# Performance work log

Hardware: AMD Instinct MI355X
Metric: run time of the kernel (lower is better)

Reference implementation:

```python
import jax, jax.numpy as jnp
import numpy as np

N = 50000      # nodes
E = 800000     # edges (avg degree 16)
D = 128        # d_model
H = 8          # num_heads
DK = D // H    # d_k = 16


def setup_inputs() -> dict:
    key = jax.random.key(0)
    ks = jax.random.split(key, 9)
    scale = np.float32(1.0 / np.sqrt(D))
    return {
        "q": jax.random.normal(ks[0], (N, D), jnp.float32),
        "k": jax.random.normal(ks[1], (N, D), jnp.float32),
        "v": jax.random.normal(ks[2], (N, D), jnp.float32),
        "e": jax.random.normal(ks[3], (E, D), jnp.float32),
        "src": jax.random.randint(ks[4], (E,), 0, N),
        "dst": jax.random.randint(ks[5], (E,), 0, N),
        # nn.Linear(D, D, bias=False) weights, stored as [in, out]
        "Wq": jax.random.normal(ks[6], (D, D), jnp.float32) * scale,
        "Wk": jax.random.normal(ks[7], (D, D), jnp.float32) * scale,
        "Wv": jax.random.normal(ks[8], (D, D), jnp.float32) * scale,
    }


def reference(q, k, v, e, src, dst, Wq, Wk, Wv):
    inv_sqrt_dk = np.float32(1.0 / np.sqrt(DK))
    # node-level V projection, then per-edge gather of src V  -> [E, H, DK]
    Vn = (v @ Wv).reshape(N, H, DK)
    Ve = Vn[src]
    # per-edge Q from dst node, K from (src k + edge feature e)
    Qe = (q[dst] @ Wq).reshape(E, H, DK)
    Ke = ((k[src] + e) @ Wk).reshape(E, H, DK)
    # per-edge HxH score matrix: Q @ K^T / sqrt(d_k), leaky-relu
    s = jnp.einsum("ehd,egd->ehg", Qe, Ke) * inv_sqrt_dk   # [E, H, H]
    s = jax.nn.leaky_relu(s)
    # softmax over last head axis (within each edge, as in reduce_func dim=-1)
    A = jax.nn.softmax(s, axis=-1)
    # per-edge message, heads regrouped -> [E, D]
    He = jnp.einsum("ehg,egd->ehd", A, Ve).reshape(E, D)
    # plain sum over incoming edges per destination node -> [N, D]
    return jax.ops.segment_sum(He, dst, num_segments=N)
```

## Files before the change

kernel.cpp:

```cpp
#include <hip/hip_runtime.h>
#include <hip/hip_bf16.h>
#include <math.h>

#define NN 50000
#define EE 800000
#define DD 128
#define HH 8
#define DKK 16

typedef __attribute__((ext_vector_type(8))) short short8;
typedef __attribute__((ext_vector_type(4))) float f32x4;
typedef __attribute__((ext_vector_type(4))) unsigned short ushort4v;
typedef __attribute__((ext_vector_type(8))) unsigned short ushort8v;

static __device__ __forceinline__ unsigned short f2bf(float x) {
  __hip_bfloat16 h = __float2bfloat16(x);
  return *reinterpret_cast<unsigned short*>(&h);
}
static __device__ __forceinline__ float bf2f(unsigned short u) {
  return __uint_as_float(((unsigned int)u) << 16);
}

__global__ __launch_bounds__(256) void hist_kernel(const int* __restrict__ dst,
                                                   int* __restrict__ cnt) {
  int i4 = blockIdx.x * 256 + threadIdx.x;
  if (i4 < EE / 4) {
    int4 d = *(const int4*)&dst[i4 * 4];
    atomicAdd(&cnt[d.x], 1);
    atomicAdd(&cnt[d.y], 1);
    atomicAdd(&cnt[d.z], 1);
    atomicAdd(&cnt[d.w], 1);
  }
}

#define SCAN_NB ((NN + 1023) / 1024)

__global__ __launch_bounds__(256) void scan1_kernel(const int* __restrict__ cnt,
                                                    int* __restrict__ bsum) {
  __shared__ int red[256];
  const int b = blockIdx.x, t = threadIdx.x;
  const int base = b * 1024 + t * 4;
  int s = 0;
  if (base + 3 < NN) {
    int4 v = *(const int4*)&cnt[base];
    s = v.x + v.y + v.z + v.w;
  } else {
    for (int j = 0; j < 4; ++j) if (base + j < NN) s += cnt[base + j];
  }
  red[t] = s;
  __syncthreads();
  for (int off = 1; off < 256; off <<= 1) {
    int v = (t >= off) ? red[t - off] : 0;
    __syncthreads();
    red[t] += v;
    __syncthreads();
  }
  if (t == 255) bsum[b] = red[255];
}

__global__ __launch_bounds__(256) void scan3_kernel(const int* __restrict__ cnt,
                                                    const int* __restrict__ bsum,
                                                    int* __restrict__ rowptr) {
  __shared__ int red[256];
  __shared__ int bs[SCAN_NB];
  const int b = blockIdx.x, t = threadIdx.x;
  if (t < SCAN_NB) bs[t] = bsum[t];
  const int base = b * 1024 + t * 4;
  int v0 = 0, v1 = 0, v2 = 0, v3 = 0;
  if (base + 3 < NN) {
    int4 v = *(const int4*)&cnt[base];
    v0 = v.x; v1 = v.y; v2 = v.z; v3 = v.w;
  } else {
    if (base + 0 < NN) v0 = cnt[base + 0];
    if (base + 1 < NN) v1 = cnt[base + 1];
    if (base + 2 < NN) v2 = cnt[base + 2];
    if (base + 3 < NN) v3 = cnt[base + 3];
  }
  red[t] = v0 + v1 + v2 + v3;
  __syncthreads();
  for (int off = 1; off < 256; off <<= 1) {
    int v = (t >= off) ? red[t - off] : 0;
    __syncthreads();
    red[t] += v;
    __syncthreads();
  }
  int bpre = 0;
  for (int j = 0; j < b; ++j) bpre += bs[j];
  int r = bpre + ((t == 0) ? 0 : red[t - 1]);
  if (base + 0 < NN) { rowptr[base + 0] = r; r += v0; }
  if (base + 1 < NN) { rowptr[base + 1] = r; r += v1; }
  if (base + 2 < NN) { rowptr[base + 2] = r; r += v2; }
  if (base + 3 < NN) { rowptr[base + 3] = r; }
}

__global__ __launch_bounds__(256) void fill_kernel(const int* __restrict__ dst,
                                                   const int* __restrict__ rowptr,
                                                   int* __restrict__ cur,
                                                   int* __restrict__ perm) {
  int i4 = blockIdx.x * 256 + threadIdx.x;
  if (i4 < EE / 4) {
    int4 dv = *(const int4*)&dst[i4 * 4];
    int d0 = dv.x, d1 = dv.y, d2 = dv.z, d3 = dv.w;
    int s0 = atomicAdd(&cur[d0], 1); perm[rowptr[d0] + s0] = i4 * 4 + 0;
    int s1 = atomicAdd(&cur[d1], 1); perm[rowptr[d1] + s1] = i4 * 4 + 1;
    int s2 = atomicAdd(&cur[d2], 1); perm[rowptr[d2] + s2] = i4 * 4 + 2;
    int s3 = atomicAdd(&cur[d3], 1); perm[rowptr[d3] + s3] = i4 * 4 + 3;
  }
}

__global__ void prep_w_kernel(const float* __restrict__ Wq,
                              const float* __restrict__ Wk,
                              const float* __restrict__ Wv,
                              unsigned short* __restrict__ WqT,
                              unsigned short* __restrict__ WkT,
                              unsigned short* __restrict__ WvT) {
  int c = blockIdx.x & 127;
  int m = blockIdx.x >> 7;
  int j = threadIdx.x;
  const float* W = (m == 0) ? Wq : (m == 1) ? Wk : Wv;
  unsigned short* o = (m == 0) ? WqT : (m == 1) ? WkT : WvT;
  o[j * DD + c] = f2bf(W[c * DD + j]);
}

__global__ __launch_bounds__(512) void node_proj_kernel(
    const float* __restrict__ q, const float* __restrict__ v,
    const float* __restrict__ k,
    const unsigned short* __restrict__ WqT, const unsigned short* __restrict__ WvT,
    unsigned short* __restrict__ Qh, unsigned short* __restrict__ Vh,
    unsigned short* __restrict__ kh)
{
  __shared__ __align__(16) unsigned short xl[64 * 136];
  const int tid = threadIdx.x;
  const int n0 = blockIdx.x * 64;

  #pragma unroll
  for (int p = 0; p < 2; ++p) {
    int f = p * 512 + tid;
    int i = f >> 4, c8 = f & 15;
    int n = n0 + i;
    if (n < NN) {
      float4 a = *(const float4*)&k[(size_t)n * DD + c8 * 8];
      float4 b = *(const float4*)&k[(size_t)n * DD + c8 * 8 + 4];
      ushort8v o = { f2bf(a.x), f2bf(a.y), f2bf(a.z), f2bf(a.w),
                     f2bf(b.x), f2bf(b.y), f2bf(b.z), f2bf(b.w) };
      *(ushort8v*)&kh[(size_t)n * DD + c8 * 8] = o;
    }
  }

  for (int m = 0; m < 2; ++m) {
    const float* x = m ? v : q;
    const unsigned short* WT = m ? WvT : WqT;
    unsigned short* o = m ? Vh : Qh;

    __syncthreads();
    #pragma unroll
    for (int p = 0; p < 4; ++p) {
      int f = p * 512 + tid;
      int i = f >> 5, c4 = f & 31;
      int n = n0 + i;
      float4 t = (n < NN) ? *(const float4*)&x[(size_t)n * DD + c4 * 4]
                          : float4{0.f, 0.f, 0.f, 0.f};
      ushort4v u = { f2bf(t.x), f2bf(t.y), f2bf(t.z), f2bf(t.w) };
      *(ushort4v*)&xl[i * 136 + c4 * 4] = u;
    }
    __syncthreads();

    const int lane = tid & 63, wid = tid >> 6;
    const int rg = wid & 3, cg = wid >> 2;
    const int lr = lane & 15, lg = lane >> 4;

    f32x4 acc0 = {0.f,0.f,0.f,0.f}, acc1 = {0.f,0.f,0.f,0.f};
    f32x4 acc2 = {0.f,0.f,0.f,0.f}, acc3 = {0.f,0.f,0.f,0.f};

    const unsigned short* Ab = &xl[(rg * 16 + lr) * 136];
    const unsigned short* B0 = &WT[(size_t)(cg * 64 +  0 + lr) * DD];
    const unsigned short* B1 = &WT[(size_t)(cg * 64 + 16 + lr) * DD];
    const unsigned short* B2 = &WT[(size_t)(cg * 64 + 32 + lr) * DD];
    const unsigned short* B3 = &WT[(size_t)(cg * 64 + 48 + lr) * DD];

    #pragma unroll
    for (int kk = 0; kk < 4; ++kk) {
      const int kof = kk * 32 + lg * 8;
      short8 a = *(const short8*)(Ab + kof);
      acc0 = __builtin_amdgcn_mfma_f32_16x16x32_bf16(a, *(const short8*)(B0 + kof), acc0, 0, 0, 0);
      acc1 = __builtin_amdgcn_mfma_f32_16x16x32_bf16(a, *(const short8*)(B1 + kof), acc1, 0, 0, 0);
      acc2 = __builtin_amdgcn_mfma_f32_16x16x32_bf16(a, *(const short8*)(B2 + kof), acc2, 0, 0, 0);
      acc3 = __builtin_amdgcn_mfma_f32_16x16x32_bf16(a, *(const short8*)(B3 + kof), acc3, 0, 0, 0);
    }

    const int r0 = rg * 16 + lg * 4;
    const int cb = cg * 64 + lr;
    #pragma unroll
    for (int r = 0; r < 4; ++r) {
      int n = n0 + r0 + r;
      if (n < NN) {
        unsigned short* orow = &o[(size_t)n * DD + cb];
        orow[ 0] = f2bf(acc0[r]);
        orow[16] = f2bf(acc1[r]);
        orow[32] = f2bf(acc2[r]);
        orow[48] = f2bf(acc3[r]);
      }
    }
  }
}

__global__ __launch_bounds__(512) void edge_attn_kernel(
    const unsigned short* __restrict__ kh, const float* __restrict__ e,
    const int* __restrict__ src, const int* __restrict__ dst,
    const int* __restrict__ perm,
    const unsigned short* __restrict__ WkT,
    const unsigned short* __restrict__ Qh, const unsigned short* __restrict__ Vh,
    float* __restrict__ out)
{
  __shared__ __align__(16) unsigned short buf[64 * 136];
  __shared__ __align__(16) unsigned short vbuf[64 * 136];
  __shared__ __align__(16) unsigned short pbuf[8 * 16 * 24];
  __shared__ int s_perm[64], s_src[64], s_dst[64];

  const int tid = threadIdx.x;
  const size_t e0 = (size_t)blockIdx.x * 64;
  const int lane = tid & 63, wid = tid >> 6;
  const int lr = lane & 15, lg = lane >> 4;

  if (tid < 64) {
    int pe = perm[e0 + tid];
    s_perm[tid] = pe;
    s_src[tid] = src[pe];
    s_dst[tid] = dst[pe];
  }
  __syncthreads();

  #pragma unroll
  for (int p = 0; p < 2; ++p) {
    int f = p * 512 + tid;
    int i2 = f >> 4, c8 = f & 15;
    ushort8v vv = *(const ushort8v*)&Vh[(size_t)s_src[i2] * DD + c8 * 8];
    ushort8v kv = *(const ushort8v*)&kh[(size_t)s_src[i2] * DD + c8 * 8];
    const float* ep = &e[(size_t)s_perm[i2] * DD + c8 * 8];
    float4 ea = *(const float4*)ep;
    float4 eb = *(const float4*)(ep + 4);
    *(ushort8v*)&vbuf[i2 * 136 + c8 * 8] = vv;
    ushort8v o;
    o[0] = f2bf(bf2f(kv[0]) + ea.x);
    o[1] = f2bf(bf2f(kv[1]) + ea.y);
    o[2] = f2bf(bf2f(kv[2]) + ea.z);
    o[3] = f2bf(bf2f(kv[3]) + ea.w);
    o[4] = f2bf(bf2f(kv[4]) + eb.x);
    o[5] = f2bf(bf2f(kv[5]) + eb.y);
    o[6] = f2bf(bf2f(kv[6]) + eb.z);
    o[7] = f2bf(bf2f(kv[7]) + eb.w);
    *(ushort8v*)&buf[i2 * 136 + c8 * 8] = o;
  }

  const short8 zero8 = {0, 0, 0, 0, 0, 0, 0, 0};
  const int ebase = wid * 8;
  short8 qf[4];
  #pragma unroll
  for (int j = 0; j < 4; ++j) {
    if (lg < 2) {
      int ie = ebase + 2 * j + (lr >> 3);
      qf[j] = *(const short8*)&Qh[(size_t)s_dst[ie] * DD + (lr & 7) * DKK + lg * 8];
    } else qf[j] = zero8;
  }
  __syncthreads();

  {
    const int rg = wid & 3, cg = wid >> 2;

    f32x4 a0 = {0.f,0.f,0.f,0.f}, a1 = {0.f,0.f,0.f,0.f};
    f32x4 a2 = {0.f,0.f,0.f,0.f}, a3 = {0.f,0.f,0.f,0.f};

    const unsigned short* Ab = &buf[(rg * 16 + lr) * 136];
    const unsigned short* B0 = &WkT[(size_t)(cg * 64 +  0 + lr) * DD];
    const unsigned short* B1 = &WkT[(size_t)(cg * 64 + 16 + lr) * DD];
    const unsigned short* B2 = &WkT[(size_t)(cg * 64 + 32 + lr) * DD];
    const unsigned short* B3 = &WkT[(size_t)(cg * 64 + 48 + lr) * DD];

    #pragma unroll
    for (int kk = 0; kk < 4; ++kk) {
      const int kof = kk * 32 + lg * 8;
      short8 a = *(const short8*)(Ab + kof);
      a0 = __builtin_amdgcn_mfma_f32_16x16x32_bf16(a, *(const short8*)(B0 + kof), a0, 0, 0, 0);
      a1 = __builtin_amdgcn_mfma_f32_16x16x32_bf16(a, *(const short8*)(B1 + kof), a1, 0, 0, 0);
      a2 = __builtin_amdgcn_mfma_f32_16x16x32_bf16(a, *(const short8*)(B2 + kof), a2, 0, 0, 0);
      a3 = __builtin_amdgcn_mfma_f32_16x16x32_bf16(a, *(const short8*)(B3 + kof), a3, 0, 0, 0);
    }

    __syncthreads();

    const int r0 = rg * 16 + lg * 4;
    const int cb = cg * 64 + lr;
    #pragma unroll
    for (int r = 0; r < 4; ++r) {
      buf[(r0 + r) * 136 + cb +  0] = f2bf(a0[r]);
      buf[(r0 + r) * 136 + cb + 16] = f2bf(a1[r]);
      buf[(r0 + r) * 136 + cb + 32] = f2bf(a2[r]);
      buf[(r0 + r) * 136 + cb + 48] = f2bf(a3[r]);
    }
  }
  __syncthreads();

  {
    const bool valid = ((lr < 8) == (lg < 2));
    unsigned short* pb = &pbuf[wid * 16 * 24];

    #pragma unroll
    for (int j = 0; j < 4; ++j) {
      const int iea = ebase + 2 * j, ieb = iea + 1;

      short8 af = zero8;
      if (lg < 2) {
        int ie = (lr < 8) ? iea : ieb;
        af = *(const short8*)&buf[ie * 136 + (lr & 7) * DKK + lg * 8];
      }
      f32x4 c = {0.f, 0.f, 0.f, 0.f};
      c = __builtin_amdgcn_mfma_f32_16x16x32_bf16(af, qf[j], c, 0, 0, 0);

      float s0, s1, s2, s3;
      {
        float x0 = c[0] * 0.25f, x1 = c[1] * 0.25f;
        float x2 = c[2] * 0.25f, x3 = c[3] * 0.25f;
        x0 = (x0 >= 0.f) ? x0 : 0.01f * x0;
        x1 = (x1 >= 0.f) ? x1 : 0.01f * x1;
        x2 = (x2 >= 0.f) ? x2 : 0.01f * x2;
        x3 = (x3 >= 0.f) ? x3 : 0.01f * x3;
        s0 = valid ? x0 : -1e30f;
        s1 = valid ? x1 : -1e30f;
        s2 = valid ? x2 : -1e30f;
        s3 = valid ? x3 : -1e30f;
      }
      float m = fmaxf(fmaxf(s0, s1), fmaxf(s2, s3));
      m = fmaxf(m, __shfl_xor(m, 16));
      m = fmaxf(m, __shfl_xor(m, 32));
      float p0 = __expf(s0 - m), p1 = __expf(s1 - m);
      float p2 = __expf(s2 - m), p3 = __expf(s3 - m);
      float su = p0 + p1 + p2 + p3;
      su += __shfl_xor(su, 16);
      su += __shfl_xor(su, 32);
      float rs = 1.0f / su;

      ushort4v pk = { f2bf(p0 * rs), f2bf(p1 * rs), f2bf(p2 * rs), f2bf(p3 * rs) };
      *(ushort4v*)&pb[lr * 24 + lg * 4] = pk;

      short8 pa = zero8;
      if (lg < 2) pa = *(const short8*)&pb[lr * 24 + lg * 8];
      short8 vf = zero8;
      if (lg < 2) {
        const unsigned short* vr = &vbuf[(lg ? ieb : iea) * 136 + lr];
        vf[0] = (short)vr[0 * 16];
        vf[1] = (short)vr[1 * 16];
        vf[2] = (short)vr[2 * 16];
        vf[3] = (short)vr[3 * 16];
        vf[4] = (short)vr[4 * 16];
        vf[5] = (short)vr[5 * 16];
        vf[6] = (short)vr[6 * 16];
        vf[7] = (short)vr[7 * 16];
      }
      f32x4 hc = {0.f, 0.f, 0.f, 0.f};
      hc = __builtin_amdgcn_mfma_f32_16x16x32_bf16(pa, vf, hc, 0, 0, 0);

      #pragma unroll
      for (int r = 0; r < 4; ++r) {
        int rr = lg * 4 + r;
        int ie = (rr < 8) ? iea : ieb;
        buf[ie * 136 + (rr & 7) * DKK + lr] = f2bf(hc[r]);
      }
    }
  }

  {
    const int d2 = lane;
    float s0 = 0.0f, s1 = 0.0f;
    int curd = s_dst[ebase];
    #pragma unroll 8
    for (int j = 0; j < 8; ++j) {
      int i2 = ebase + j;
      int dn2 = s_dst[i2];
      if (dn2 != curd) {
        atomicAdd(&out[(size_t)curd * DD + d2 * 2],     s0);
        atomicAdd(&out[(size_t)curd * DD + d2 * 2 + 1], s1);
        s0 = 0.0f; s1 = 0.0f;
        curd = dn2;
      }
      unsigned int w = *(const unsigned int*)&buf[i2 * 136 + d2 * 2];
      s0 += bf2f((unsigned short)(w & 0xffff));
      s1 += bf2f((unsigned short)(w >> 16));
    }
    atomicAdd(&out[(size_t)curd * DD + d2 * 2],     s0);
    atomicAdd(&out[(size_t)curd * DD + d2 * 2 + 1], s1);
  }
}

extern "C" void kernel_launch(void* const* d_in, const int* in_sizes, int n_in,
                              void* d_out, int out_size, void* d_ws, size_t ws_size,
                              hipStream_t stream) {
  const float* q  = (const float*)d_in[0];
  const float* k  = (const float*)d_in[1];
  const float* v  = (const float*)d_in[2];
  const float* e  = (const float*)d_in[3];
  const int*   src = (const int*)d_in[4];
  const int*   dst = (const int*)d_in[5];
  const float* Wq = (const float*)d_in[6];
  const float* Wk = (const float*)d_in[7];
  const float* Wv = (const float*)d_in[8];

  float* out = (float*)d_out;
  char* wsb = (char*)d_ws;
  unsigned short* Qh  = (unsigned short*)wsb;
  unsigned short* Vh  = Qh + (size_t)NN * DD;
  unsigned short* kh  = Vh + (size_t)NN * DD;
  unsigned short* WqT = kh + (size_t)NN * DD;
  unsigned short* WkT = WqT + DD * DD;
  unsigned short* WvT = WkT + DD * DD;
  int* cnt    = (int*)(WvT + DD * DD);
  int* cur    = cnt + NN;
  int* rowptr = cur + NN;
  int* bsum   = rowptr + NN + 1;
  int* perm   = bsum + 64;

  hipMemsetAsync(d_out, 0, (size_t)NN * DD * sizeof(float), stream);
  hipMemsetAsync(cnt, 0, 2 * NN * sizeof(int), stream);

  hist_kernel <<<(EE / 4 + 255) / 256, 256, 0, stream>>>(dst, cnt);
  scan1_kernel<<<SCAN_NB, 256, 0, stream>>>(cnt, bsum);
  scan3_kernel<<<SCAN_NB, 256, 0, stream>>>(cnt, bsum, rowptr);
  fill_kernel <<<(EE / 4 + 255) / 256, 256, 0, stream>>>(dst, rowptr, cur, perm);

  prep_w_kernel<<<3 * DD, DD, 0, stream>>>(Wq, Wk, Wv, WqT, WkT, WvT);
  node_proj_kernel<<<(NN + 63) / 64, 512, 0, stream>>>(q, v, k, WqT, WvT,
                                                       Qh, Vh, kh);
  edge_attn_kernel<<<EE / 64, 512, 0, stream>>>(kh, e, src, dst, perm,
                                                WkT, Qh, Vh, out);
}
```

Measured before the change: 416.2 us.

## Stage edge features via direct global-to-LDS loads and read V straight from global

Edge feature rows are now copied into a shared-memory float buffer with global_load_lds, so the bulk e traffic bypasses registers. The k loads and Q fragment loads are issued before the barrier so they overlap with that transfer. The V staging buffer is removed and V fragments are gathered directly from global memory in the attention step. The final segment reduction now has each thread handle one column over 16 edges after a new barrier, which changes the granularity of the atomic adds. In exchange, LDS use rises with the fp32 e buffer, and the direct V gathers are strided 2-byte global reads.

```diff
diff --git a/kernel.cpp b/kernel.cpp
--- a/kernel.cpp
+++ b/kernel.cpp
@@ -19,6 +19,12 @@
 }
 static __device__ __forceinline__ float bf2f(unsigned short u) {
   return __uint_as_float(((unsigned int)u) << 16);
+}
+
+static __device__ __forceinline__ void gload_lds16(void* lds, const void* g) {
+  __builtin_amdgcn_global_load_lds(
+      (const __attribute__((address_space(1))) unsigned int*)g,
+      (__attribute__((address_space(3))) unsigned int*)lds, 16, 0, 0);
 }
 
 __global__ __launch_bounds__(256) void hist_kernel(const int* __restrict__ dst,
@@ -213,7 +219,7 @@
     float* __restrict__ out)
 {
   __shared__ __align__(16) unsigned short buf[64 * 136];
-  __shared__ __align__(16) unsigned short vbuf[64 * 136];
+  __shared__ __align__(16) float ebuf[64 * 128];
   __shared__ __align__(16) unsigned short pbuf[8 * 16 * 24];
   __shared__ int s_perm[64], s_src[64], s_dst[64];
 
@@ -231,15 +237,40 @@
   __syncthreads();
 
   #pragma unroll
-  for (int p = 0; p < 2; ++p) {
-    int f = p * 512 + tid;
-    int i2 = f >> 4, c8 = f & 15;
-    ushort8v vv = *(const ushort8v*)&Vh[(size_t)s_src[i2] * DD + c8 * 8];
-    ushort8v kv = *(const ushort8v*)&kh[(size_t)s_src[i2] * DD + c8 * 8];
-    const float* ep = &e[(size_t)s_perm[i2] * DD + c8 * 8];
-    float4 ea = *(const float4*)ep;
-    float4 eb = *(const float4*)(ep + 4);
-    *(ushort8v*)&vbuf[i2 * 136 + c8 * 8] = vv;
+  for (int t = 0; t < 4; ++t) {
+    int ew = (wid << 3) + (t << 1) + (lane >> 5);
+    const float* gp = &e[(size_t)s_perm[ew] * DD + (lane & 31) * 4];
+    gload_lds16(&ebuf[wid * 1024 + t * 256], gp);
+  }
+
+  ushort8v kvv[2];
+  #pragma unroll
+  for (int j = 0; j < 2; ++j) {
+    int flat = j * 512 + tid;
+    kvv[j] = *(const ushort8v*)&kh[(size_t)s_src[flat >> 4] * DD + (flat & 15) * 8];
+  }
+
+  const short8 zero8 = {0, 0, 0, 0, 0, 0, 0, 0};
+  const int ebase = wid * 8;
+  short8 qf[4];
+  #pragma unroll
+  for (int j = 0; j < 4; ++j) {
+    if (lg < 2) {
+      int ie = ebase + 2 * j + (lr >> 3);
+      qf[j] = *(const short8*)&Qh[(size_t)s_dst[ie] * DD + (lr & 7) * DKK + lg * 8];
+    } else qf[j] = zero8;
+  }
+  __syncthreads();
+
+  #pragma unroll
+  for (int j = 0; j < 2; ++j) {
+    int flat = j * 512 + tid;
+    int i2 = flat >> 4, c8 = flat & 15;
+    int we = i2 >> 3, j2 = i2 & 7;
+    const float* ef = &ebuf[we * 1024 + (j2 >> 1) * 256 + (j2 & 1) * 128 + c8 * 8];
+    float4 ea = *(const float4*)ef;
+    float4 eb = *(const float4*)(ef + 4);
+    ushort8v kv = kvv[j];
     ushort8v o;
     o[0] = f2bf(bf2f(kv[0]) + ea.x);
     o[1] = f2bf(bf2f(kv[1]) + ea.y);
@@ -250,17 +281,6 @@
     o[6] = f2bf(bf2f(kv[6]) + eb.z);
     o[7] = f2bf(bf2f(kv[7]) + eb.w);
     *(ushort8v*)&buf[i2 * 136 + c8 * 8] = o;
-  }
-
-  const short8 zero8 = {0, 0, 0, 0, 0, 0, 0, 0};
-  const int ebase = wid * 8;
-  short8 qf[4];
-  #pragma unroll
-  for (int j = 0; j < 4; ++j) {
-    if (lg < 2) {
-      int ie = ebase + 2 * j + (lr >> 3);
-      qf[j] = *(const short8*)&Qh[(size_t)s_dst[ie] * DD + (lr & 7) * DKK + lg * 8];
-    } else qf[j] = zero8;
   }
   __syncthreads();
 
@@ -346,7 +366,7 @@
       if (lg < 2) pa = *(const short8*)&pb[lr * 24 + lg * 8];
       short8 vf = zero8;
       if (lg < 2) {
-        const unsigned short* vr = &vbuf[(lg ? ieb : iea) * 136 + lr];
+        const unsigned short* vr = &Vh[(size_t)s_src[lg ? ieb : iea] * DD + lr];
         vf[0] = (short)vr[0 * 16];
         vf[1] = (short)vr[1 * 16];
         vf[2] = (short)vr[2 * 16];
@@ -367,27 +387,25 @@
       }
     }
   }
+  __syncthreads();
 
   {
-    const int d2 = lane;
-    float s0 = 0.0f, s1 = 0.0f;
-    int curd = s_dst[ebase];
+    const int c = tid >> 7, d2 = tid & 127;
+    const int base = c * 16;
+    float s = 0.0f;
+    int curd = s_dst[base];
     #pragma unroll 8
-    for (int j = 0; j < 8; ++j) {
-      int i2 = ebase + j;
+    for (int j = 0; j < 16; ++j) {
+      int i2 = base + j;
       int dn2 = s_dst[i2];
       if (dn2 != curd) {
-        atomicAdd(&out[(size_t)curd * DD + d2 * 2],     s0);
-        atomicAdd(&out[(size_t)curd * DD + d2 * 2 + 1], s1);
-        s0 = 0.0f; s1 = 0.0f;
+        atomicAdd(&out[(size_t)curd * DD + d2], s);
+        s = 0.0f;
         curd = dn2;
       }
-      unsigned int w = *(const unsigned int*)&buf[i2 * 136 + d2 * 2];
-      s0 += bf2f((unsigned short)(w & 0xffff));
-      s1 += bf2f((unsigned short)(w >> 16));
-    }
-    atomicAdd(&out[(size_t)curd * DD + d2 * 2],     s0);
-    atomicAdd(&out[(size_t)curd * DD + d2 * 2 + 1], s1);
+      s += bf2f(buf[i2 * 136 + d2]);
+    }
+    atomicAdd(&out[(size_t)curd * DD + d2], s);
   }
 }
 
```

After: 493.6 us. +18.6%, slower.

## Make edge attention wave-local: each wave owns 16 edges, drop shared staging

Applied to the files above, without the earlier changes.

The edge attention kernel now runs 256 threads, and each of its 4 waves owns 16 edges end to end. Each wave loads k+e straight from global into MFMA A-fragments and computes all 128 output columns of the K projection with 8 accumulators. The V staging buffer is removed, and V fragments are gathered directly from global memory in the score/message stage. This removes shared-memory staging and two block barriers and roughly halves LDS use, which should raise occupancy. In exchange it raises register pressure, gives uncoalesced strided global V reads, and makes each wave read the full WkT.

```diff
diff --git a/kernel.cpp b/kernel.cpp
--- a/kernel.cpp
+++ b/kernel.cpp
@@ -204,7 +204,7 @@
   }
 }
 
-__global__ __launch_bounds__(512) void edge_attn_kernel(
+__global__ __launch_bounds__(256) void edge_attn_kernel(
     const unsigned short* __restrict__ kh, const float* __restrict__ e,
     const int* __restrict__ src, const int* __restrict__ dst,
     const int* __restrict__ perm,
@@ -213,14 +213,14 @@
     float* __restrict__ out)
 {
   __shared__ __align__(16) unsigned short buf[64 * 136];
-  __shared__ __align__(16) unsigned short vbuf[64 * 136];
-  __shared__ __align__(16) unsigned short pbuf[8 * 16 * 24];
+  __shared__ __align__(16) unsigned short pbuf[4 * 16 * 24];
   __shared__ int s_perm[64], s_src[64], s_dst[64];
 
   const int tid = threadIdx.x;
   const size_t e0 = (size_t)blockIdx.x * 64;
   const int lane = tid & 63, wid = tid >> 6;
   const int lr = lane & 15, lg = lane >> 4;
+  const int ebase = wid * 16;
 
   if (tid < 64) {
     int pe = perm[e0 + tid];
@@ -230,82 +230,60 @@
   }
   __syncthreads();
 
+  const short8 zero8 = {0, 0, 0, 0, 0, 0, 0, 0};
+  short8 qf[8];
   #pragma unroll
-  for (int p = 0; p < 2; ++p) {
-    int f = p * 512 + tid;
-    int i2 = f >> 4, c8 = f & 15;
-    ushort8v vv = *(const ushort8v*)&Vh[(size_t)s_src[i2] * DD + c8 * 8];
-    ushort8v kv = *(const ushort8v*)&kh[(size_t)s_src[i2] * DD + c8 * 8];
-    const float* ep = &e[(size_t)s_perm[i2] * DD + c8 * 8];
-    float4 ea = *(const float4*)ep;
-    float4 eb = *(const float4*)(ep + 4);
-    *(ushort8v*)&vbuf[i2 * 136 + c8 * 8] = vv;
-    ushort8v o;
-    o[0] = f2bf(bf2f(kv[0]) + ea.x);
-    o[1] = f2bf(bf2f(kv[1]) + ea.y);
-    o[2] = f2bf(bf2f(kv[2]) + ea.z);
-    o[3] = f2bf(bf2f(kv[3]) + ea.w);
-    o[4] = f2bf(bf2f(kv[4]) + eb.x);
-    o[5] = f2bf(bf2f(kv[5]) + eb.y);
-    o[6] = f2bf(bf2f(kv[6]) + eb.z);
-    o[7] = f2bf(bf2f(kv[7]) + eb.w);
-    *(ushort8v*)&buf[i2 * 136 + c8 * 8] = o;
-  }
-
-  const short8 zero8 = {0, 0, 0, 0, 0, 0, 0, 0};
-  const int ebase = wid * 8;
-  short8 qf[4];
-  #pragma unroll
-  for (int j = 0; j < 4; ++j) {
+  for (int j = 0; j < 8; ++j) {
     if (lg < 2) {
       int ie = ebase + 2 * j + (lr >> 3);
       qf[j] = *(const short8*)&Qh[(size_t)s_dst[ie] * DD + (lr & 7) * DKK + lg * 8];
     } else qf[j] = zero8;
   }
-  __syncthreads();
 
   {
-    const int rg = wid & 3, cg = wid >> 2;
-
-    f32x4 a0 = {0.f,0.f,0.f,0.f}, a1 = {0.f,0.f,0.f,0.f};
-    f32x4 a2 = {0.f,0.f,0.f,0.f}, a3 = {0.f,0.f,0.f,0.f};
-
-    const unsigned short* Ab = &buf[(rg * 16 + lr) * 136];
-    const unsigned short* B0 = &WkT[(size_t)(cg * 64 +  0 + lr) * DD];
-    const unsigned short* B1 = &WkT[(size_t)(cg * 64 + 16 + lr) * DD];
-    const unsigned short* B2 = &WkT[(size_t)(cg * 64 + 32 + lr) * DD];
-    const unsigned short* B3 = &WkT[(size_t)(cg * 64 + 48 + lr) * DD];
+    const int prow = s_perm[ebase + lr];
+    const int srow = s_src[ebase + lr];
+    const unsigned short* khp = &kh[(size_t)srow * DD];
+    const float* ep = &e[(size_t)prow * DD];
+
+    f32x4 acc[8];
+    #pragma unroll
+    for (int c = 0; c < 8; ++c) acc[c] = f32x4{0.f, 0.f, 0.f, 0.f};
 
     #pragma unroll
     for (int kk = 0; kk < 4; ++kk) {
       const int kof = kk * 32 + lg * 8;
-      short8 a = *(const short8*)(Ab + kof);
-      a0 = __builtin_amdgcn_mfma_f32_16x16x32_bf16(a, *(const short8*)(B0 + kof), a0, 0, 0, 0);
-      a1 = __builtin_amdgcn_mfma_f32_16x16x32_bf16(a, *(const short8*)(B1 + kof), a1, 0, 0, 0);
-      a2 = __builtin_amdgcn_mfma_f32_16x16x32_bf16(a, *(const short8*)(B2 + kof), a2, 0, 0, 0);
-      a3 = __builtin_amdgcn_mfma_f32_16x16x32_bf16(a, *(const short8*)(B3 + kof), a3, 0, 0, 0);
-    }
-
-    __syncthreads();
-
-    const int r0 = rg * 16 + lg * 4;
-    const int cb = cg * 64 + lr;
-    #pragma unroll
-    for (int r = 0; r < 4; ++r) {
-      buf[(r0 + r) * 136 + cb +  0] = f2bf(a0[r]);
-      buf[(r0 + r) * 136 + cb + 16] = f2bf(a1[r]);
-      buf[(r0 + r) * 136 + cb + 32] = f2bf(a2[r]);
-      buf[(r0 + r) * 136 + cb + 48] = f2bf(a3[r]);
-    }
-  }
-  __syncthreads();
+      ushort8v kv = *(const ushort8v*)(khp + kof);
+      float4 ea = *(const float4*)(ep + kof);
+      float4 eb = *(const float4*)(ep + kof + 4);
+      short8 af;
+      af[0] = (short)f2bf(bf2f(kv[0]) + ea.x);
+      af[1] = (short)f2bf(bf2f(kv[1]) + ea.y);
+      af[2] = (short)f2bf(bf2f(kv[2]) + ea.z);
+      af[3] = (short)f2bf(bf2f(kv[3]) + ea.w);
+      af[4] = (short)f2bf(bf2f(kv[4]) + eb.x);
+      af[5] = (short)f2bf(bf2f(kv[5]) + eb.y);
+      af[6] = (short)f2bf(bf2f(kv[6]) + eb.z);
+      af[7] = (short)f2bf(bf2f(kv[7]) + eb.w);
+      #pragma unroll
+      for (int c = 0; c < 8; ++c) {
+        short8 bf = *(const short8*)&WkT[(size_t)(c * 16 + lr) * DD + kof];
+        acc[c] = __builtin_amdgcn_mfma_f32_16x16x32_bf16(af, bf, acc[c], 0, 0, 0);
+      }
+    }
+    #pragma unroll
+    for (int c = 0; c < 8; ++c)
+      #pragma unroll
+      for (int r = 0; r < 4; ++r)
+        buf[(ebase + lg * 4 + r) * 136 + c * 16 + lr] = f2bf(acc[c][r]);
+  }
 
   {
     const bool valid = ((lr < 8) == (lg < 2));
     unsigned short* pb = &pbuf[wid * 16 * 24];
 
     #pragma unroll
-    for (int j = 0; j < 4; ++j) {
+    for (int j = 0; j < 8; ++j) {
       const int iea = ebase + 2 * j, ieb = iea + 1;
 
       short8 af = zero8;
@@ -346,7 +324,7 @@
       if (lg < 2) pa = *(const short8*)&pb[lr * 24 + lg * 8];
       short8 vf = zero8;
       if (lg < 2) {
-        const unsigned short* vr = &vbuf[(lg ? ieb : iea) * 136 + lr];
+        const unsigned short* vr = &Vh[(size_t)s_src[lg ? ieb : iea] * DD + lr];
         vf[0] = (short)vr[0 * 16];
         vf[1] = (short)vr[1 * 16];
         vf[2] = (short)vr[2 * 16];
@@ -373,7 +351,7 @@
     float s0 = 0.0f, s1 = 0.0f;
     int curd = s_dst[ebase];
     #pragma unroll 8
-    for (int j = 0; j < 8; ++j) {
+    for (int j = 0; j < 16; ++j) {
       int i2 = ebase + j;
       int dn2 = s_dst[i2];
       if (dn2 != curd) {
@@ -429,6 +407,6 @@
   prep_w_kernel<<<3 * DD, DD, 0, stream>>>(Wq, Wk, Wv, WqT, WkT, WvT);
   node_proj_kernel<<<(NN + 63) / 64, 512, 0, stream>>>(q, v, k, WqT, WvT,
                                                        Qh, Vh, kh);
-  edge_attn_kernel<<<EE / 64, 512, 0, stream>>>(kh, e, src, dst, perm,
+  edge_attn_kernel<<<EE / 64, 256, 0, stream>>>(kh, e, src, dst, perm,
                                                 WkT, Qh, Vh, out);
 }
```

Measured after the change: 535.2 us. +28.6%, slower.
